# Kernel tuning notes

Hardware: AMD Instinct MI355X
Metric: run time of the kernel (lower is better)

## Reference

```python
import jax, jax.numpy as jnp
import numpy as np

# MSDeformAttn dims inferred from Linear shapes: 8 heads * 4 levels * 2 points
H, L, P, D, C = 8, 4, 2, 32, 256
SHAPES = [(128, 128), (64, 64), (32, 32), (16, 16)]  # (H_l, W_l) per level
NV = sum(h * w for h, w in SHAPES)  # 21760
STARTS = np.cumsum([0] + [h * w for h, w in SHAPES])


def _bilinear(val, lx, ly, Hl, Wl):
    """grid_sample(align_corners=False, padding='zeros') equivalent.
    val: [B, H, Hl*Wl, D]; lx, ly: [B, H, N] normalized sample coords in [0,1].
    Returns [B, H, N, D]."""
    x = lx * Wl - 0.5
    y = ly * Hl - 0.5
    x0 = jnp.floor(x)
    y0 = jnp.floor(y)
    fx = x - x0
    fy = y - y0
    x0i = x0.astype(jnp.int32)
    y0i = y0.astype(jnp.int32)
    out = jnp.zeros(val.shape[:2] + (x.shape[-1], val.shape[-1]), val.dtype)
    corners = ((0, 0, (1 - fx) * (1 - fy)), (1, 0, fx * (1 - fy)),
               (0, 1, (1 - fx) * fy), (1, 1, fx * fy))
    for dx, dy, w in corners:
        xi = x0i + dx
        yi = y0i + dy
        valid = ((xi >= 0) & (xi < Wl) & (yi >= 0) & (yi < Hl)).astype(val.dtype)
        idx = jnp.clip(yi, 0, Hl - 1) * Wl + jnp.clip(xi, 0, Wl - 1)
        g = jnp.take_along_axis(val, idx[..., None], axis=2)  # [B,H,N,D]
        out = out + g * (w * valid)[..., None]
    return out


def setup_inputs() -> dict:
    key = jax.random.key(0)
    ks = jax.random.split(key, 8)
    B, NQ = 4, 1000
    s = 0.02
    return {
        "query": jax.random.normal(ks[0], (B, NQ, C), jnp.float32),
        "value": jax.random.normal(ks[1], (B, NV, C), jnp.float32),
        "reference_points": jax.random.uniform(ks[2], (B, NQ, L, 2), jnp.float32),
        "W_off": jax.random.normal(ks[3], (C, H * L * P * 2), jnp.float32) * s,
        "b_off": jnp.zeros((H * L * P * 2,), jnp.float32),
        "W_attn": jax.random.normal(ks[4], (C, H * L * P), jnp.float32) * s,
        "b_attn": jnp.zeros((H * L * P,), jnp.float32),
        "W_val": jax.random.normal(ks[5], (C, C), jnp.float32) * s,
        "b_val": jnp.zeros((C,), jnp.float32),
        "W_out": jax.random.normal(ks[6], (C, C), jnp.float32) * s,
        "b_out": jnp.zeros((C,), jnp.float32),
    }


def reference(query, value, reference_points, W_off, b_off, W_attn, b_attn,
              W_val, b_val, W_out, b_out):
    B, NQ, _ = query.shape
    # value projection -> per-head values [B, H, NV, D]
    v = (value @ W_val + b_val).reshape(B, NV, H, D).transpose(0, 2, 1, 3)
    # sampling offsets [B, NQ, H, L, P, 2]
    off = (query @ W_off + b_off).reshape(B, NQ, H, L, P, 2)
    # attention weights: softmax over L*P
    attn = jax.nn.softmax((query @ W_attn + b_attn).reshape(B, NQ, H, L * P), axis=-1)
    attn = attn.reshape(B, NQ, H, L, P)
    # normalizer (W_l, H_l) per level, matching Deformable-DETR
    wh = jnp.asarray([[w, h] for h, w in SHAPES], dtype=query.dtype)  # [L,2]
    loc = reference_points[:, :, None, :, None, :] + off / wh[None, None, None, :, None, :]
    out = jnp.zeros((B, H, NQ, D), dtype=query.dtype)
    for l, (hl, wl) in enumerate(SHAPES):
        vl = v[:, :, STARTS[l]:STARTS[l + 1], :]                 # [B,H,hl*wl,D]
        lx = loc[:, :, :, l, :, 0].transpose(0, 2, 1, 3).reshape(B, H, NQ * P)
        ly = loc[:, :, :, l, :, 1].transpose(0, 2, 1, 3).reshape(B, H, NQ * P)
        s = _bilinear(vl, lx, ly, hl, wl).reshape(B, H, NQ, P, D)
        al = attn[:, :, :, l, :].transpose(0, 2, 1, 3)           # [B,H,NQ,P]
        out = out + jnp.sum(s * al[..., None], axis=3)
    out = out.transpose(0, 2, 1, 3).reshape(B, NQ, C)
    return out @ W_out + b_out  # dropout(p=0) is identity
```

## Files before the change

### kernel.cpp

```cpp
#include <hip/hip_runtime.h>

#define HH 8
#define LL 4
#define PP 2
#define DD 32
#define CC 256
#define NVV 21760
#define NQQ 1000
#define BB 4
#define NQT (BB * NQQ)

typedef __attribute__((ext_vector_type(8))) short short8;
typedef __attribute__((ext_vector_type(4))) short shortv4;
typedef __attribute__((ext_vector_type(4))) float f32x4;

__device__ __forceinline__ unsigned short f2bf(float f) {
    unsigned u = __float_as_uint(f);
    u += 0x7FFF + ((u >> 16) & 1);
    return (unsigned short)(u >> 16);
}
__device__ __forceinline__ float bf2f(unsigned short h) {
    return __uint_as_float(((unsigned)h) << 16);
}
__device__ __forceinline__ unsigned cvtpk(float lo, float hi) {
    unsigned r;
    asm volatile("v_cvt_pk_bf16_f32 %0, %1, %2" : "=v"(r) : "v"(lo), "v"(hi));
    return r;
}

__device__ __forceinline__ void gload_lds16(const void* g, void* l) {
    __builtin_amdgcn_global_load_lds(
        (const __attribute__((address_space(1))) unsigned int*)g,
        (__attribute__((address_space(3))) unsigned int*)l, 16, 0, 0);
}

__global__ __launch_bounds__(256) void prep_kernel(
    const float* __restrict__ Wv, const float* __restrict__ Woff,
    const float* __restrict__ Wattn, const float* __restrict__ Wout,
    unsigned short* __restrict__ WTs, unsigned short* __restrict__ W1T,
    unsigned short* __restrict__ WoT)
{
    const int c = blockIdx.x;
    const int n = threadIdx.x;
    {
        int s = c >> 5, t = c & 31;
        WTs[s * 8192 + n * 32 + (t ^ (((n >> 1) & 3) << 3))] =
            f2bf(Wv[c * CC + n]);
    }
    if (n < 192) {
        float x = (n < 128) ? Woff[c * 128 + n] : Wattn[c * 64 + (n - 128)];
        W1T[n * CC + c] = f2bf(x);
    }
    WoT[n * CC + c] = f2bf(Wout[c * CC + n]);
}

__global__ __launch_bounds__(256, 3) void valproj_mfma(
    const float* __restrict__ value, const unsigned short* __restrict__ WTs,
    const float* __restrict__ bv, unsigned short* __restrict__ v_out)
{
    __shared__ __align__(16) char Abuf[2][8192];
    __shared__ __align__(16) char Bbuf[2][16384];

    const int tid = threadIdx.x;
    const int lane = tid & 63;
    const int w = tid >> 6;
    const int wm = w >> 1;
    const int wn = w & 1;
    const int lr = lane & 15;
    const int q = lane >> 4;
    const int bm = blockIdx.x * 64;

#define STAGE(s, bi)                                                        \
    {                                                                       \
        _Pragma("unroll") for (int r = 0; r < 2; ++r) {                     \
            int u = r * 256 + tid;                                          \
            int m = u >> 3, c = u & 7;                                      \
            gload_lds16((const char*)value + (size_t)(bm + m) * 1024 +      \
                            (s) * 128 + ((c ^ (m & 7)) * 16),               \
                        &Abuf[bi][u * 16]);                                 \
        }                                                                   \
        _Pragma("unroll") for (int r = 0; r < 4; ++r) {                     \
            int off = (r * 256 + tid) * 16;                                 \
            gload_lds16((const char*)WTs + (s) * 16384 + off,               \
                        &Bbuf[bi][off]);                                    \
        }                                                                   \
    }

    f32x4 acc[2][8] = {};

    STAGE(0, 0);
    __syncthreads();

#pragma unroll
    for (int s = 0; s < 8; ++s) {
        const int cur = s & 1;
        if (s < 7) STAGE(s + 1, cur ^ 1);

        short8 af[2];
#pragma unroll
        for (int mf = 0; mf < 2; ++mf) {
            int m = wm * 32 + mf * 16 + lr;
            const char* base = &Abuf[cur][m * 128];
            f32x4 lo = *(const f32x4*)(base + (((2 * q) ^ (m & 7)) * 16));
            f32x4 hi = *(const f32x4*)(base + (((2 * q + 1) ^ (m & 7)) * 16));
            uint4 uv = {cvtpk(lo[0], lo[1]), cvtpk(lo[2], lo[3]),
                        cvtpk(hi[0], hi[1]), cvtpk(hi[2], hi[3])};
            af[mf] = __builtin_bit_cast(short8, uv);
        }
#pragma unroll
        for (int nf = 0; nf < 8; ++nf) {
            int n = wn * 128 + nf * 16 + lr;
            short8 bf = *(const short8*)&Bbuf[cur][n * 64 +
                                                   ((q ^ ((n >> 1) & 3)) * 16)];
            acc[0][nf] = __builtin_amdgcn_mfma_f32_16x16x32_bf16(
                af[0], bf, acc[0][nf], 0, 0, 0);
            acc[1][nf] = __builtin_amdgcn_mfma_f32_16x16x32_bf16(
                af[1], bf, acc[1][nf], 0, 0, 0);
        }
        __syncthreads();
    }
#undef STAGE

#pragma unroll
    for (int nf = 0; nf < 8; ++nf) {
        int col = wn * 128 + nf * 16 + lr;
        float bias = bv[col];
#pragma unroll
        for (int mf = 0; mf < 2; ++mf) {
            size_t rbase = (size_t)(bm + wm * 32 + mf * 16 + q * 4) * 256 + col;
#pragma unroll
            for (int r = 0; r < 4; ++r)
                v_out[rbase + (size_t)r * 256] = f2bf(acc[mf][nf][r] + bias);
        }
    }
}

__global__ __launch_bounds__(256) void logits_mfma(
    const float* __restrict__ query, const unsigned short* __restrict__ W1T,
    const float* __restrict__ b_off, const float* __restrict__ b_attn,
    float* __restrict__ logits)
{
    __shared__ unsigned short As[32][72];
    __shared__ unsigned short Bsl[192][72];
    const int tid = threadIdx.x;
    const int lane = tid & 63;
    const int wave = tid >> 6;
    const int bm = blockIdx.x * 32;
    const int lr = lane & 15;
    const int q = lane >> 4;
    f32x4 acc[2][3] = {};

    for (int k0 = 0; k0 < CC; k0 += 64) {
        float4 a[2];
        short8 wv[6];
#pragma unroll
        for (int i = 0; i < 2; ++i) {
            int u = tid + 256 * i;
            a[i] = *(const float4*)&query[(size_t)(bm + (u >> 4)) * CC + k0 +
                                          (u & 15) * 4];
        }
#pragma unroll
        for (int i = 0; i < 6; ++i) {
            int u = tid + 256 * i;
            wv[i] = *(const short8*)&W1T[(size_t)(u >> 3) * CC + k0 + (u & 7) * 8];
        }
        __syncthreads();
#pragma unroll
        for (int i = 0; i < 2; ++i) {
            int u = tid + 256 * i;
            shortv4 p;
            p[0] = (short)f2bf(a[i].x); p[1] = (short)f2bf(a[i].y);
            p[2] = (short)f2bf(a[i].z); p[3] = (short)f2bf(a[i].w);
            *(shortv4*)&As[u >> 4][(u & 15) * 4] = p;
        }
#pragma unroll
        for (int i = 0; i < 6; ++i) {
            int u = tid + 256 * i;
            *(short8*)&Bsl[u >> 3][(u & 7) * 8] = wv[i];
        }
        __syncthreads();

#pragma unroll
        for (int kk = 0; kk < 2; ++kk) {
            short8 afr[2], bfr[3];
#pragma unroll
            for (int mf = 0; mf < 2; ++mf)
                afr[mf] = *(const short8*)&As[mf * 16 + lr][kk * 32 + q * 8];
#pragma unroll
            for (int nf = 0; nf < 3; ++nf)
                bfr[nf] =
                    *(const short8*)&Bsl[wave * 48 + nf * 16 + lr][kk * 32 + q * 8];
#pragma unroll
            for (int mf = 0; mf < 2; ++mf)
#pragma unroll
                for (int nf = 0; nf < 3; ++nf)
                    acc[mf][nf] = __builtin_amdgcn_mfma_f32_16x16x32_bf16(
                        afr[mf], bfr[nf], acc[mf][nf], 0, 0, 0);
        }
        __syncthreads();
    }

#pragma unroll
    for (int nf = 0; nf < 3; ++nf) {
        int col = wave * 48 + nf * 16 + lr;
        float bias = (col < 128) ? b_off[col] : b_attn[col - 128];
#pragma unroll
        for (int mf = 0; mf < 2; ++mf)
#pragma unroll
            for (int r = 0; r < 4; ++r) {
                int m = bm + mf * 16 + q * 4 + r;
                logits[(size_t)m * 192 + col] = acc[mf][nf][r] + bias;
            }
    }
}

__global__ __launch_bounds__(256) void sample_kernel(
    const float* __restrict__ logits,
    const float* __restrict__ refp,
    const unsigned short* __restrict__ v,
    unsigned short* __restrict__ mid)
{
    __shared__ float offl[128];
    __shared__ float attnl[64];
    __shared__ float refl[8];

    const int qy = blockIdx.x;
    const int b = qy / NQQ;
    const int tid = threadIdx.x;

    if (tid < 192) {
        float t = logits[(size_t)qy * 192 + tid];
        if (tid < 128) offl[tid] = t;
        else attnl[tid - 128] = t;
    } else if (tid < 200) {
        refl[tid - 192] = refp[(size_t)qy * 8 + (tid - 192)];
    }
    __syncthreads();

    if (tid < 8) {
        float m = -1e30f;
#pragma unroll
        for (int j = 0; j < 8; ++j) m = fmaxf(m, attnl[tid * 8 + j]);
        float s = 0.f, e[8];
#pragma unroll
        for (int j = 0; j < 8; ++j) {
            e[j] = __expf(attnl[tid * 8 + j] - m);
            s += e[j];
        }
        float inv = 1.f / s;
#pragma unroll
        for (int j = 0; j < 8; ++j) attnl[tid * 8 + j] = e[j] * inv;
    }
    __syncthreads();

    const int h = tid >> 5, d = tid & 31;
    const int starts[4] = {0, 16384, 20480, 21504};
    const float szs[4] = {128.f, 64.f, 32.f, 16.f};

    float acc = 0.f;
#pragma unroll
    for (int l = 0; l < LL; ++l) {
        const float S = szs[l];
        const int Wl = (int)S;
        const float refx = refl[l * 2 + 0];
        const float refy = refl[l * 2 + 1];
        const unsigned short* vl =
            v + (size_t)(b * NVV + starts[l]) * 256 + h * 32 + d;
#pragma unroll
        for (int p = 0; p < PP; ++p) {
            const int oi = h * 16 + l * 4 + p * 2;
            float lx = refx + offl[oi + 0] / S;
            float ly = refy + offl[oi + 1] / S;
            float x = lx * S - 0.5f;
            float y = ly * S - 0.5f;
            float x0f = floorf(x), y0f = floorf(y);
            float fx = x - x0f, fy = y - y0f;
            int x0 = (int)x0f, y0 = (int)y0f;
            float a = attnl[h * 8 + l * 2 + p];
            float sacc = 0.f;
#pragma unroll
            for (int dy = 0; dy < 2; ++dy) {
#pragma unroll
                for (int dx = 0; dx < 2; ++dx) {
                    int xi = x0 + dx, yi = y0 + dy;
                    float wgt = (dx ? fx : 1.f - fx) * (dy ? fy : 1.f - fy);
                    bool valid = (xi >= 0) && (xi < Wl) && (yi >= 0) && (yi < Wl);
                    int xc = min(max(xi, 0), Wl - 1);
                    int yc = min(max(yi, 0), Wl - 1);
                    float g = bf2f(vl[(size_t)(yc * Wl + xc) * 256]);
                    sacc += g * (valid ? wgt : 0.f);
                }
            }
            acc += a * sacc;
        }
    }
    mid[(size_t)qy * CC + h * 32 + d] = f2bf(acc);
}

__global__ __launch_bounds__(256) void out_mfma(
    const unsigned short* __restrict__ mid,
    const unsigned short* __restrict__ WoT, const float* __restrict__ b_out,
    float* __restrict__ out)
{
    __shared__ unsigned short As[32][72];
    __shared__ unsigned short Bso[256][72];
    const int tid = threadIdx.x;
    const int lane = tid & 63;
    const int wave = tid >> 6;
    const int bm = blockIdx.x * 32;
    const int lr = lane & 15;
    const int q = lane >> 4;
    f32x4 acc[2][4] = {};

    for (int k0 = 0; k0 < CC; k0 += 64) {
        short8 a0 = *(const short8*)&mid[(size_t)(bm + (tid >> 3)) * CC + k0 +
                                         (tid & 7) * 8];
        short8 wv[8];
#pragma unroll
        for (int i = 0; i < 8; ++i) {
            int u = tid + 256 * i;
            wv[i] = *(const short8*)&WoT[(size_t)(u >> 3) * CC + k0 + (u & 7) * 8];
        }
        __syncthreads();
        *(short8*)&As[tid >> 3][(tid & 7) * 8] = a0;
#pragma unroll
        for (int i = 0; i < 8; ++i) {
            int u = tid + 256 * i;
            *(short8*)&Bso[u >> 3][(u & 7) * 8] = wv[i];
        }
        __syncthreads();

#pragma unroll
        for (int kk = 0; kk < 2; ++kk) {
            short8 afr[2], bfr[4];
#pragma unroll
            for (int mf = 0; mf < 2; ++mf)
                afr[mf] = *(const short8*)&As[mf * 16 + lr][kk * 32 + q * 8];
#pragma unroll
            for (int nf = 0; nf < 4; ++nf)
                bfr[nf] =
                    *(const short8*)&Bso[wave * 64 + nf * 16 + lr][kk * 32 + q * 8];
#pragma unroll
            for (int mf = 0; mf < 2; ++mf)
#pragma unroll
                for (int nf = 0; nf < 4; ++nf)
                    acc[mf][nf] = __builtin_amdgcn_mfma_f32_16x16x32_bf16(
                        afr[mf], bfr[nf], acc[mf][nf], 0, 0, 0);
        }
        __syncthreads();
    }

#pragma unroll
    for (int nf = 0; nf < 4; ++nf) {
        int col = wave * 64 + nf * 16 + lr;
        float bias = b_out[col];
#pragma unroll
        for (int mf = 0; mf < 2; ++mf)
#pragma unroll
            for (int r = 0; r < 4; ++r) {
                int m = bm + mf * 16 + q * 4 + r;
                out[(size_t)m * CC + col] = acc[mf][nf][r] + bias;
            }
    }
}

extern "C" void kernel_launch(void* const* d_in, const int* in_sizes, int n_in,
                              void* d_out, int out_size, void* d_ws, size_t ws_size,
                              hipStream_t stream) {
    const float* query  = (const float*)d_in[0];
    const float* value  = (const float*)d_in[1];
    const float* refp   = (const float*)d_in[2];
    const float* W_off  = (const float*)d_in[3];
    const float* b_off  = (const float*)d_in[4];
    const float* W_attn = (const float*)d_in[5];
    const float* b_attn = (const float*)d_in[6];
    const float* W_val  = (const float*)d_in[7];
    const float* b_val  = (const float*)d_in[8];
    const float* W_out  = (const float*)d_in[9];
    const float* b_out  = (const float*)d_in[10];
    float* out = (float*)d_out;

    char* ws = (char*)d_ws;
    unsigned short* WTs    = (unsigned short*)(ws);
    unsigned short* v_ws   = (unsigned short*)(ws + 131072);
    unsigned short* W1T    = (unsigned short*)(ws + 44695552);
    unsigned short* WoT    = (unsigned short*)(ws + 44793856);
    float*          logits = (float*)(ws + 44924928);
    unsigned short* mid    = (unsigned short*)(ws + 47996928);

    prep_kernel<<<CC, 256, 0, stream>>>(W_val, W_off, W_attn, W_out,
                                        WTs, W1T, WoT);
    valproj_mfma<<<(BB * NVV) / 64, 256, 0, stream>>>(value, WTs, b_val, v_ws);
    logits_mfma<<<NQT / 32, 256, 0, stream>>>(query, W1T, b_off, b_attn, logits);
    sample_kernel<<<NQT, 256, 0, stream>>>(logits, refp, v_ws, mid);
    out_mfma<<<NQT / 32, 256, 0, stream>>>(mid, WoT, b_out, out);
}
```

Measured before the change: 63.84 us.

## Keep value-projection weights in registers and loop over row tiles per block

```diff
diff --git a/kernel.cpp b/kernel.cpp
--- a/kernel.cpp
+++ b/kernel.cpp
@@ -37,16 +37,12 @@
 __global__ __launch_bounds__(256) void prep_kernel(
     const float* __restrict__ Wv, const float* __restrict__ Woff,
     const float* __restrict__ Wattn, const float* __restrict__ Wout,
-    unsigned short* __restrict__ WTs, unsigned short* __restrict__ W1T,
+    unsigned short* __restrict__ WT, unsigned short* __restrict__ W1T,
     unsigned short* __restrict__ WoT)
 {
     const int c = blockIdx.x;
     const int n = threadIdx.x;
-    {
-        int s = c >> 5, t = c & 31;
-        WTs[s * 8192 + n * 32 + (t ^ (((n >> 1) & 3) << 3))] =
-            f2bf(Wv[c * CC + n]);
-    }
+    WT[n * CC + c] = f2bf(Wv[c * CC + n]);
     if (n < 192) {
         float x = (n < 128) ? Woff[c * 128 + n] : Wattn[c * 64 + (n - 128)];
         W1T[n * CC + c] = f2bf(x);
@@ -54,85 +50,88 @@
     WoT[n * CC + c] = f2bf(Wout[c * CC + n]);
 }
 
-__global__ __launch_bounds__(256, 3) void valproj_mfma(
-    const float* __restrict__ value, const unsigned short* __restrict__ WTs,
+__global__ __launch_bounds__(512, 4) void valproj_mfma(
+    const float* __restrict__ value, const unsigned short* __restrict__ WT,
     const float* __restrict__ bv, unsigned short* __restrict__ v_out)
 {
-    __shared__ __align__(16) char Abuf[2][8192];
-    __shared__ __align__(16) char Bbuf[2][16384];
+    __shared__ __align__(16) char Abuf[2][32768];
 
     const int tid = threadIdx.x;
     const int lane = tid & 63;
     const int w = tid >> 6;
-    const int wm = w >> 1;
-    const int wn = w & 1;
     const int lr = lane & 15;
     const int q = lane >> 4;
-    const int bm = blockIdx.x * 64;
-
-#define STAGE(s, bi)                                                        \
+    const int t0 = blockIdx.x * 5;
+
+    short8 breg[2][8];
+    float bias[2];
+#pragma unroll
+    for (int cf = 0; cf < 2; ++cf) {
+        int col = w * 32 + cf * 16 + lr;
+        bias[cf] = bv[col];
+#pragma unroll
+        for (int s = 0; s < 8; ++s)
+            breg[cf][s] = *(const short8*)&WT[(size_t)col * CC + s * 32 + q * 8];
+    }
+
+#define STAGE_A(tg, bi)                                                     \
     {                                                                       \
-        _Pragma("unroll") for (int r = 0; r < 2; ++r) {                     \
-            int u = r * 256 + tid;                                          \
-            int m = u >> 3, c = u & 7;                                      \
-            gload_lds16((const char*)value + (size_t)(bm + m) * 1024 +      \
-                            (s) * 128 + ((c ^ (m & 7)) * 16),               \
+        _Pragma("unroll") for (int r = 0; r < 4; ++r) {                     \
+            int u = r * 512 + tid;                  \
+            int m = u >> 6, c = u & 63;                                     \
+            gload_lds16((const char*)value + (size_t)(tg) * 32768 +         \
+                            m * 1024 + ((c ^ (m & 7)) * 16),                \
                         &Abuf[bi][u * 16]);                                 \
         }                                                                   \
-        _Pragma("unroll") for (int r = 0; r < 4; ++r) {                     \
-            int off = (r * 256 + tid) * 16;                                 \
-            gload_lds16((const char*)WTs + (s) * 16384 + off,               \
-                        &Bbuf[bi][off]);                                    \
-        }                                                                   \
-    }
-
-    f32x4 acc[2][8] = {};
-
-    STAGE(0, 0);
+    }
+
+    STAGE_A(t0, 0);
     __syncthreads();
 
 #pragma unroll
-    for (int s = 0; s < 8; ++s) {
-        const int cur = s & 1;
-        if (s < 7) STAGE(s + 1, cur ^ 1);
-
-        short8 af[2];
-#pragma unroll
-        for (int mf = 0; mf < 2; ++mf) {
-            int m = wm * 32 + mf * 16 + lr;
-            const char* base = &Abuf[cur][m * 128];
-            f32x4 lo = *(const f32x4*)(base + (((2 * q) ^ (m & 7)) * 16));
-            f32x4 hi = *(const f32x4*)(base + (((2 * q + 1) ^ (m & 7)) * 16));
-            uint4 uv = {cvtpk(lo[0], lo[1]), cvtpk(lo[2], lo[3]),
-                        cvtpk(hi[0], hi[1]), cvtpk(hi[2], hi[3])};
-            af[mf] = __builtin_bit_cast(short8, uv);
-        }
-#pragma unroll
-        for (int nf = 0; nf < 8; ++nf) {
-            int n = wn * 128 + nf * 16 + lr;
-            short8 bf = *(const short8*)&Bbuf[cur][n * 64 +
-                                                   ((q ^ ((n >> 1) & 3)) * 16)];
-            acc[0][nf] = __builtin_amdgcn_mfma_f32_16x16x32_bf16(
-                af[0], bf, acc[0][nf], 0, 0, 0);
-            acc[1][nf] = __builtin_amdgcn_mfma_f32_16x16x32_bf16(
-                af[1], bf, acc[1][nf], 0, 0, 0);
-        }
-        __syncthreads();
-    }
-#undef STAGE
-
-#pragma unroll
-    for (int nf = 0; nf < 8; ++nf) {
-        int col = wn * 128 + nf * 16 + lr;
-        float bias = bv[col];
-#pragma unroll
-        for (int mf = 0; mf < 2; ++mf) {
-            size_t rbase = (size_t)(bm + wm * 32 + mf * 16 + q * 4) * 256 + col;
-#pragma unroll
-            for (int r = 0; r < 4; ++r)
-                v_out[rbase + (size_t)r * 256] = f2bf(acc[mf][nf][r] + bias);
-        }
-    }
+    for (int t = 0; t < 5; ++t) {
+        const int cur = t & 1;
+        if (t < 4) STAGE_A(t0 + t + 1, cur ^ 1);
+
+        f32x4 acc[2][2] = {};
+#pragma unroll
+        for (int s = 0; s < 8; ++s) {
+            short8 af[2];
+#pragma unroll
+            for (int rf = 0; rf < 2; ++rf) {
+                int row = rf * 16 + lr;
+                const char* base = &Abuf[cur][row * 1024];
+                int ch = s * 8 + q * 2;
+                f32x4 lo = *(const f32x4*)(base + ((ch ^ (row & 7)) * 16));
+                f32x4 hi = *(const f32x4*)(base + (((ch + 1) ^ (row & 7)) * 16));
+                uint4 uv = {cvtpk(lo[0], lo[1]), cvtpk(lo[2], lo[3]),
+                            cvtpk(hi[0], hi[1]), cvtpk(hi[2], hi[3])};
+                af[rf] = __builtin_bit_cast(short8, uv);
+            }
+#pragma unroll
+            for (int rf = 0; rf < 2; ++rf)
+#pragma unroll
+                for (int cf = 0; cf < 2; ++cf)
+                    acc[rf][cf] = __builtin_amdgcn_mfma_f32_16x16x32_bf16(
+                        af[rf], breg[cf][s], acc[rf][cf], 0, 0, 0);
+        }
+
+        const int trow = (t0 + t) * 32;
+#pragma unroll
+        for (int rf = 0; rf < 2; ++rf)
+#pragma unroll
+            for (int r = 0; r < 4; ++r) {
+                size_t rbase = (size_t)(trow + rf * 16 + q * 4 + r) * 256;
+#pragma unroll
+                for (int cf = 0; cf < 2; ++cf) {
+                    int col = w * 32 + cf * 16 + lr;
+                    v_out[rbase + col] = f2bf(acc[rf][cf][r] + bias[cf]);
+                }
+            }
+
+        __syncthreads();
+    }
+#undef STAGE_A
 }
 
 __global__ __launch_bounds__(256) void logits_mfma(
@@ -381,7 +380,7 @@
     float* out = (float*)d_out;
 
     char* ws = (char*)d_ws;
-    unsigned short* WTs    = (unsigned short*)(ws);
+    unsigned short* WT     = (unsigned short*)(ws);
     unsigned short* v_ws   = (unsigned short*)(ws + 131072);
     unsigned short* W1T    = (unsigned short*)(ws + 44695552);
     unsigned short* WoT    = (unsigned short*)(ws + 44793856);
@@ -389,8 +388,8 @@
     unsigned short* mid    = (unsigned short*)(ws + 47996928);
 
     prep_kernel<<<CC, 256, 0, stream>>>(W_val, W_off, W_attn, W_out,
-                                        WTs, W1T, WoT);
-    valproj_mfma<<<(BB * NVV) / 64, 256, 0, stream>>>(value, WTs, b_val, v_ws);
+                                        WT, W1T, WoT);
+    valproj_mfma<<<544, 512, 0, stream>>>(value, WT, b_val, v_ws);
     logits_mfma<<<NQT / 32, 256, 0, stream>>>(query, W1T, b_off, b_attn, logits);
     sample_kernel<<<NQT, 256, 0, stream>>>(logits, refp, v_ws, mid);
     out_mfma<<<NQT / 32, 256, 0, stream>>>(mid, WoT, b_out, out);
```

Result: slower. 70.15 us (+9.9%).
